# Performance work log

Measured on AMD Instinct MI355X. Metric: run time of the kernel, lower is better.

The kernel has to match this reference:

```python
import jax, jax.numpy as jnp
import numpy as np

EPS = 1e-08
SLOPE = 0.01  # LeakyReLU default negative_slope
B = 2097152
H = 32

def leaky_relu(x):
    return jnp.where(x >= 0, x, SLOPE * x)

def gram_schmidt(v, w):
    # v, w: [b,3]
    v_on = v / (jnp.linalg.norm(v, axis=-1, keepdims=True) + EPS)
    proj = jnp.sum(w * v_on, axis=-1, keepdims=True) * v_on
    w_orth = w - proj
    w_on = w_orth / (jnp.linalg.norm(w_orth, axis=-1, keepdims=True) + EPS)
    u_on = jnp.cross(v_on, w_on)
    R = jnp.stack((v_on, w_on, u_on), axis=-1)  # [b,3,3]
    v_local = jnp.einsum('bji,bj->bi', R, v)    # R^T @ v
    w_local = jnp.einsum('bji,bj->bi', R, w)
    return R, v_local, w_local

def setup_inputs() -> dict:
    key = jax.random.key(0)
    ks = jax.random.split(key, 12)
    std = 0.0001  # init_weights() normal std
    return {
        'v': jax.random.normal(ks[0], (B, 3), jnp.float32),
        'w': jax.random.normal(ks[1], (B, 3), jnp.float32),
        'W1': jax.random.normal(ks[2], (H, 3), jnp.float32) * std,
        'b1': jax.random.normal(ks[3], (H,), jnp.float32) * std,
        'W2': jax.random.normal(ks[4], (H, H), jnp.float32) * std,
        'b2': jax.random.normal(ks[5], (H,), jnp.float32) * std,
        'Wd1': jax.random.normal(ks[6], (H, H), jnp.float32) * std,
        'bd1': jax.random.normal(ks[7], (H,), jnp.float32) * std,
        'Wd2': jax.random.normal(ks[8], (3, H), jnp.float32) * std,
        'bd2': jax.random.normal(ks[9], (3,), jnp.float32) * std,
        'bias': jnp.array([[0.0, 0.0, -9.81]], jnp.float32),
    }

def reference(v, w, W1, b1, W2, b2, Wd1, bd1, Wd2, bd2, bias):
    shapes = v.shape
    b = shapes[0]
    v = v.reshape(b, 3)
    w = w.reshape(b, 3)
    R, v_local, w_local = gram_schmidt(v, w)
    feat = jnp.concatenate([v_local[..., :1], w_local[..., :2]], axis=-1)  # [b,3]
    h1 = leaky_relu(feat @ W1.T + b1)           # [b,H]
    h = leaky_relu(h1 @ W2.T + b2) * h1         # [b,H]
    y = leaky_relu(h @ Wd1.T + bd1) @ Wd2.T + bd2  # [b,3]
    y = jnp.einsum('bij,bj->bi', R, y) + bias
    return y.reshape(shapes)
```

## Files before the change

### kernel.cpp

```cpp
#include <hip/hip_runtime.h>
#include <math.h>

typedef __attribute__((ext_vector_type(8))) short short8;
typedef __attribute__((ext_vector_type(4))) float f32x4;
typedef __attribute__((ext_vector_type(4))) unsigned int u32x4;
typedef __attribute__((ext_vector_type(2))) unsigned long long u64x2;

static __device__ __forceinline__ unsigned int fbits(float f) {
    union { float f; unsigned int u; } v; v.f = f; return v.u;
}
static __device__ __forceinline__ float bitsf(unsigned int u) {
    union { float f; unsigned int u; } v; v.u = u; return v.f;
}
static __device__ __forceinline__ unsigned int pkbf(float lo, float hi) {
    return (fbits(hi) & 0xFFFF0000u) | (fbits(lo) >> 16);
}
static __device__ __forceinline__ float bflo(unsigned int u) { return bitsf(u << 16); }
static __device__ __forceinline__ float bfhi(unsigned int u) { return bitsf(u & 0xFFFF0000u); }
static __device__ __forceinline__ float leaky(float x) { return fmaxf(x, 0.01f * x); }


__global__ __launch_bounds__(256, 4) void aero_mfma(
    const float* __restrict__ vin, const float* __restrict__ win,
    const float* __restrict__ gW1, const float* __restrict__ gb1,
    const float* __restrict__ gW2, const float* __restrict__ gb2,
    const float* __restrict__ gWd1, const float* __restrict__ gbd1,
    const float* __restrict__ gWd2, const float* __restrict__ gbd2,
    const float* __restrict__ gbias,
    float* __restrict__ out, int nrows)
{
    __shared__ unsigned long long hbuf[256 * 9];
    __shared__ unsigned long long zbuf[256 * 9];
    unsigned int* const z32 = (unsigned int*)zbuf;

    const int tid = threadIdx.x;
    int row = blockIdx.x * 256 + tid;
    if (row >= nrows) row = nrows - 1;

    const int i15   = tid & 15;
    const int quad  = (tid >> 4) & 3;
    const int wbase = tid & 192;

    unsigned int bw2[2][4], bwd1[2][4];
    float b2v[2], bd1v[2];
    #pragma unroll
    for (int u = 0; u < 2; ++u) {
        const int n = u * 16 + i15;
        const float* p2 = gW2  + n * 32 + 4 * quad;
        const float* p3 = gWd1 + n * 32 + 4 * quad;
        #pragma unroll
        for (int j = 0; j < 4; ++j) {
            bw2[u][j]  = pkbf(p2[j], p2[j + 16]);
            bwd1[u][j] = pkbf(p3[j], p3[j + 16]);
        }
        b2v[u]  = gb2[n];
        bd1v[u] = gbd1[n];
    }

    const float v0 = vin[3 * row + 0], v1 = vin[3 * row + 1], v2 = vin[3 * row + 2];
    const float w0 = win[3 * row + 0], w1 = win[3 * row + 1], w2 = win[3 * row + 2];

    const float nv  = sqrtf(v0 * v0 + v1 * v1 + v2 * v2) + 1e-8f;
    const float rnv = 1.0f / nv;
    const float a0 = v0 * rnv, a1 = v1 * rnv, a2 = v2 * rnv;
    const float proj = w0 * a0 + w1 * a1 + w2 * a2;
    const float o0 = w0 - proj * a0, o1 = w1 - proj * a1, o2 = w2 - proj * a2;
    const float nw  = sqrtf(o0 * o0 + o1 * o1 + o2 * o2) + 1e-8f;
    const float rnw = 1.0f / nw;
    const float c0 = o0 * rnw, c1 = o1 * rnw, c2 = o2 * rnw;
    const float u0 = a1 * c2 - a2 * c1;
    const float u1 = a2 * c0 - a0 * c2;
    const float u2 = a0 * c1 - a1 * c0;

    const float f0 = v0 * a0 + v1 * a1 + v2 * a2;
    const float f1 = proj;
    const float f2 = w0 * c0 + w1 * c1 + w2 * c2;

    float h1[32];
    #pragma unroll
    for (int j = 0; j < 32; ++j) {
        float acc = gb1[j];
        acc = fmaf(gW1[3 * j + 0], f0, acc);
        acc = fmaf(gW1[3 * j + 1], f1, acc);
        acc = fmaf(gW1[3 * j + 2], f2, acc);
        h1[j] = leaky(acc);
    }

    {
        unsigned long long* dst = hbuf + tid * 9;
        #pragma unroll
        for (int c2 = 0; c2 < 8; ++c2) {
            const unsigned int lo = pkbf(h1[2 * c2],     h1[2 * c2 + 16]);
            const unsigned int hi = pkbf(h1[2 * c2 + 1], h1[2 * c2 + 17]);
            dst[c2] = (unsigned long long)lo | ((unsigned long long)hi << 32);
        }
    }

    __syncthreads();
    {
        const short8 bf0 = __builtin_bit_cast(short8, (u32x4){bw2[0][0], bw2[0][1], bw2[0][2], bw2[0][3]});
        const short8 bf1 = __builtin_bit_cast(short8, (u32x4){bw2[1][0], bw2[1][1], bw2[1][2], bw2[1][3]});
        #pragma unroll
        for (int t = 0; t < 4; ++t) {
            const int ra = wbase + 16 * t + i15;
            u64x2 av;
            av.x = hbuf[ra * 9 + 2 * quad];
            av.y = hbuf[ra * 9 + 2 * quad + 1];
            const short8 af = __builtin_bit_cast(short8, av);
            f32x4 acc0 = {b2v[0], b2v[0], b2v[0], b2v[0]};
            f32x4 acc1 = {b2v[1], b2v[1], b2v[1], b2v[1]};
            acc0 = __builtin_amdgcn_mfma_f32_16x16x32_bf16(af, bf0, acc0, 0, 0, 0);
            acc1 = __builtin_amdgcn_mfma_f32_16x16x32_bf16(af, bf1, acc1, 0, 0, 0);
            const int zr = wbase + 16 * t + 4 * quad;
            #pragma unroll
            for (int r = 0; r < 4; ++r)
                z32[(zr + r) * 18 + i15] = pkbf(acc0[r], acc1[r]);
        }
    }

    __syncthreads();
    {
        const unsigned long long* src = zbuf + tid * 9;
        unsigned long long* dst = hbuf + tid * 9;
        #pragma unroll
        for (int c2 = 0; c2 < 8; ++c2) {
            const unsigned long long zz = src[c2];
            const unsigned int ulo = (unsigned int)zz;
            const unsigned int uhi = (unsigned int)(zz >> 32);
            const float g0 = leaky(bflo(ulo)) * h1[2 * c2];
            const float g1 = leaky(bfhi(ulo)) * h1[2 * c2 + 16];
            const float g2 = leaky(bflo(uhi)) * h1[2 * c2 + 1];
            const float g3 = leaky(bfhi(uhi)) * h1[2 * c2 + 17];
            const unsigned int lo = pkbf(g0, g1);
            const unsigned int hi = pkbf(g2, g3);
            dst[c2] = (unsigned long long)lo | ((unsigned long long)hi << 32);
        }
    }

    __syncthreads();
    {
        const short8 bf0 = __builtin_bit_cast(short8, (u32x4){bwd1[0][0], bwd1[0][1], bwd1[0][2], bwd1[0][3]});
        const short8 bf1 = __builtin_bit_cast(short8, (u32x4){bwd1[1][0], bwd1[1][1], bwd1[1][2], bwd1[1][3]});
        #pragma unroll
        for (int t = 0; t < 4; ++t) {
            const int ra = wbase + 16 * t + i15;
            u64x2 av;
            av.x = hbuf[ra * 9 + 2 * quad];
            av.y = hbuf[ra * 9 + 2 * quad + 1];
            const short8 af = __builtin_bit_cast(short8, av);
            f32x4 acc0 = {bd1v[0], bd1v[0], bd1v[0], bd1v[0]};
            f32x4 acc1 = {bd1v[1], bd1v[1], bd1v[1], bd1v[1]};
            acc0 = __builtin_amdgcn_mfma_f32_16x16x32_bf16(af, bf0, acc0, 0, 0, 0);
            acc1 = __builtin_amdgcn_mfma_f32_16x16x32_bf16(af, bf1, acc1, 0, 0, 0);
            const int zr = wbase + 16 * t + 4 * quad;
            #pragma unroll
            for (int r = 0; r < 4; ++r)
                z32[(zr + r) * 18 + i15] = pkbf(acc0[r], acc1[r]);
        }
    }

    __syncthreads();
    {
        const unsigned long long* src = zbuf + tid * 9;
        float h3[32];
        #pragma unroll
        for (int c2 = 0; c2 < 8; ++c2) {
            const unsigned long long zz = src[c2];
            const unsigned int ulo = (unsigned int)zz;
            const unsigned int uhi = (unsigned int)(zz >> 32);
            h3[2 * c2]      = leaky(bflo(ulo));
            h3[2 * c2 + 16] = leaky(bfhi(ulo));
            h3[2 * c2 + 1]  = leaky(bflo(uhi));
            h3[2 * c2 + 17] = leaky(bfhi(uhi));
        }

        float y0 = gbd2[0], y1 = gbd2[1], y2 = gbd2[2];
        #pragma unroll
        for (int k = 0; k < 32; ++k) {
            y0 = fmaf(gWd2[0 * 32 + k], h3[k], y0);
            y1 = fmaf(gWd2[1 * 32 + k], h3[k], y1);
            y2 = fmaf(gWd2[2 * 32 + k], h3[k], y2);
        }

        out[3 * row + 0] = fmaf(a0, y0, fmaf(c0, y1, fmaf(u0, y2, gbias[0])));
        out[3 * row + 1] = fmaf(a1, y0, fmaf(c1, y1, fmaf(u1, y2, gbias[1])));
        out[3 * row + 2] = fmaf(a2, y0, fmaf(c2, y1, fmaf(u2, y2, gbias[2])));
    }
}

extern "C" void kernel_launch(void* const* d_in, const int* in_sizes, int n_in,
                              void* d_out, int out_size, void* d_ws, size_t ws_size,
                              hipStream_t stream) {
    const float* v    = (const float*)d_in[0];
    const float* w    = (const float*)d_in[1];
    const float* W1   = (const float*)d_in[2];
    const float* b1   = (const float*)d_in[3];
    const float* W2   = (const float*)d_in[4];
    const float* b2   = (const float*)d_in[5];
    const float* Wd1  = (const float*)d_in[6];
    const float* bd1  = (const float*)d_in[7];
    const float* Wd2  = (const float*)d_in[8];
    const float* bd2  = (const float*)d_in[9];
    const float* bias = (const float*)d_in[10];

    const int nrows = in_sizes[0] / 3;
    dim3 block(256);
    dim3 grid((nrows + 255) / 256);
    hipLaunchKernelGGL(aero_mfma, grid, block, 0, stream,
                       v, w, W1, b1, W2, b2, Wd1, bd1, Wd2, bd2, bias,
                       (float*)d_out, nrows);
}
```

Measured before the change: 141.7 us.

## Move all four MLP layers onto MFMA and fuse activations into epilogues

```diff
diff --git a/kernel.cpp b/kernel.cpp
--- a/kernel.cpp
+++ b/kernel.cpp
@@ -1,5 +1,4 @@
 #include <hip/hip_runtime.h>
-#include <math.h>
 
 typedef __attribute__((ext_vector_type(8))) short short8;
 typedef __attribute__((ext_vector_type(4))) float f32x4;
@@ -13,11 +12,15 @@
     union { float f; unsigned int u; } v; v.u = u; return v.f;
 }
 static __device__ __forceinline__ unsigned int pkbf(float lo, float hi) {
-    return (fbits(hi) & 0xFFFF0000u) | (fbits(lo) >> 16);
+    return __builtin_amdgcn_perm(fbits(hi), fbits(lo), 0x07060302u);
 }
 static __device__ __forceinline__ float bflo(unsigned int u) { return bitsf(u << 16); }
 static __device__ __forceinline__ float bfhi(unsigned int u) { return bitsf(u & 0xFFFF0000u); }
 static __device__ __forceinline__ float leaky(float x) { return fmaxf(x, 0.01f * x); }
+static __device__ __forceinline__ float rsqrt_nr(float x) {
+    const float r = __builtin_amdgcn_rsqf(x);
+    return r * (1.5f - (0.5f * x) * (r * r));
+}
 
 
 __global__ __launch_bounds__(256, 4) void aero_mfma(
@@ -31,7 +34,10 @@
 {
     __shared__ unsigned long long hbuf[256 * 9];
     __shared__ unsigned long long zbuf[256 * 9];
-    unsigned int* const z32 = (unsigned int*)zbuf;
+    __shared__ u32x4 fybuf[256];
+    unsigned int* const h32  = (unsigned int*)hbuf;
+    unsigned int* const z32  = (unsigned int*)zbuf;
+    unsigned int* const fy32 = (unsigned int*)fybuf;
 
     const int tid = threadIdx.x;
     int row = blockIdx.x * 256 + tid;
@@ -41,8 +47,8 @@
     const int quad  = (tid >> 4) & 3;
     const int wbase = tid & 192;
 
-    unsigned int bw2[2][4], bwd1[2][4];
-    float b2v[2], bd1v[2];
+    unsigned int bw1[2][4], bw2[2][4], bwd1[2][4], bwd2[4];
+    float b1v[2], b2v[2], bd1v[2];
     #pragma unroll
     for (int u = 0; u < 2; ++u) {
         const int n = u * 16 + i15;
@@ -50,56 +56,73 @@
         const float* p3 = gWd1 + n * 32 + 4 * quad;
         #pragma unroll
         for (int j = 0; j < 4; ++j) {
+            float l1 = 0.0f;
+            if (quad == 0 && j < 3) l1 = gW1[n * 3 + j];
+            bw1[u][j]  = fbits(l1) >> 16;
             bw2[u][j]  = pkbf(p2[j], p2[j + 16]);
             bwd1[u][j] = pkbf(p3[j], p3[j + 16]);
         }
+        b1v[u]  = gb1[n];
         b2v[u]  = gb2[n];
         bd1v[u] = gbd1[n];
     }
+    #pragma unroll
+    for (int j = 0; j < 4; ++j) {
+        float lo = 0.0f, hi = 0.0f;
+        if (i15 < 3) {
+            const float* p4 = gWd2 + i15 * 32 + 4 * quad;
+            lo = p4[j]; hi = p4[j + 16];
+        }
+        bwd2[j] = pkbf(lo, hi);
+    }
+    const float bd2v = (i15 < 3) ? gbd2[i15] : 0.0f;
 
     const float v0 = vin[3 * row + 0], v1 = vin[3 * row + 1], v2 = vin[3 * row + 2];
     const float w0 = win[3 * row + 0], w1 = win[3 * row + 1], w2 = win[3 * row + 2];
 
-    const float nv  = sqrtf(v0 * v0 + v1 * v1 + v2 * v2) + 1e-8f;
-    const float rnv = 1.0f / nv;
-    const float a0 = v0 * rnv, a1 = v1 * rnv, a2 = v2 * rnv;
-    const float proj = w0 * a0 + w1 * a1 + w2 * a2;
-    const float o0 = w0 - proj * a0, o1 = w1 - proj * a1, o2 = w2 - proj * a2;
-    const float nw  = sqrtf(o0 * o0 + o1 * o1 + o2 * o2) + 1e-8f;
-    const float rnw = 1.0f / nw;
-    const float c0 = o0 * rnw, c1 = o1 * rnw, c2 = o2 * rnw;
-    const float u0 = a1 * c2 - a2 * c1;
-    const float u1 = a2 * c0 - a0 * c2;
-    const float u2 = a0 * c1 - a1 * c0;
-
-    const float f0 = v0 * a0 + v1 * a1 + v2 * a2;
+    const float sv  = v0 * v0 + v1 * v1 + v2 * v2;
+    const float rnv = rsqrt_nr(sv);
+    const float vo0 = v0 * rnv, vo1 = v1 * rnv, vo2 = v2 * rnv;
+    const float proj = w0 * vo0 + w1 * vo1 + w2 * vo2;
+    const float o0 = w0 - proj * vo0, o1 = w1 - proj * vo1, o2 = w2 - proj * vo2;
+    const float sw  = o0 * o0 + o1 * o1 + o2 * o2;
+    const float rnw = rsqrt_nr(sw);
+    const float wo0 = o0 * rnw, wo1 = o1 * rnw, wo2 = o2 * rnw;
+    const float uo0 = vo1 * wo2 - vo2 * wo1;
+    const float uo1 = vo2 * wo0 - vo0 * wo2;
+    const float uo2 = vo0 * wo1 - vo1 * wo0;
+
+    const float f0 = sv * rnv;
     const float f1 = proj;
-    const float f2 = w0 * c0 + w1 * c1 + w2 * c2;
-
-    float h1[32];
-    #pragma unroll
-    for (int j = 0; j < 32; ++j) {
-        float acc = gb1[j];
-        acc = fmaf(gW1[3 * j + 0], f0, acc);
-        acc = fmaf(gW1[3 * j + 1], f1, acc);
-        acc = fmaf(gW1[3 * j + 2], f2, acc);
-        h1[j] = leaky(acc);
-    }
-
-    {
-        unsigned long long* dst = hbuf + tid * 9;
-        #pragma unroll
-        for (int c2 = 0; c2 < 8; ++c2) {
-            const unsigned int lo = pkbf(h1[2 * c2],     h1[2 * c2 + 16]);
-            const unsigned int hi = pkbf(h1[2 * c2 + 1], h1[2 * c2 + 17]);
-            dst[c2] = (unsigned long long)lo | ((unsigned long long)hi << 32);
-        }
-    }
-
-    __syncthreads();
+    const float f2 = sw * rnw;
+
+    fybuf[tid] = (u32x4){ fbits(f0) >> 16, fbits(f1) >> 16, fbits(f2) >> 16, 0u };
+    __syncthreads();
+
+    {
+        const short8 bf0 = __builtin_bit_cast(short8, (u32x4){bw1[0][0], bw1[0][1], bw1[0][2], bw1[0][3]});
+        const short8 bf1 = __builtin_bit_cast(short8, (u32x4){bw1[1][0], bw1[1][1], bw1[1][2], bw1[1][3]});
+        const f32x4 cb0 = {b1v[0], b1v[0], b1v[0], b1v[0]};
+        const f32x4 cb1 = {b1v[1], b1v[1], b1v[1], b1v[1]};
+        #pragma unroll
+        for (int t = 0; t < 4; ++t) {
+            const int ra = wbase + 16 * t + i15;
+            const short8 af = __builtin_bit_cast(short8, fybuf[ra]);
+            const f32x4 acc0 = __builtin_amdgcn_mfma_f32_16x16x32_bf16(af, bf0, cb0, 0, 0, 0);
+            const f32x4 acc1 = __builtin_amdgcn_mfma_f32_16x16x32_bf16(af, bf1, cb1, 0, 0, 0);
+            const int zr = wbase + 16 * t + 4 * quad;
+            #pragma unroll
+            for (int r = 0; r < 4; ++r)
+                h32[(zr + r) * 18 + i15] = pkbf(leaky(acc0[r]), leaky(acc1[r]));
+        }
+    }
+    __syncthreads();
+
     {
         const short8 bf0 = __builtin_bit_cast(short8, (u32x4){bw2[0][0], bw2[0][1], bw2[0][2], bw2[0][3]});
         const short8 bf1 = __builtin_bit_cast(short8, (u32x4){bw2[1][0], bw2[1][1], bw2[1][2], bw2[1][3]});
+        const f32x4 cb0 = {b2v[0], b2v[0], b2v[0], b2v[0]};
+        const f32x4 cb1 = {b2v[1], b2v[1], b2v[1], b2v[1]};
         #pragma unroll
         for (int t = 0; t < 4; ++t) {
             const int ra = wbase + 16 * t + i15;
@@ -107,40 +130,44 @@
             av.x = hbuf[ra * 9 + 2 * quad];
             av.y = hbuf[ra * 9 + 2 * quad + 1];
             const short8 af = __builtin_bit_cast(short8, av);
-            f32x4 acc0 = {b2v[0], b2v[0], b2v[0], b2v[0]};
-            f32x4 acc1 = {b2v[1], b2v[1], b2v[1], b2v[1]};
-            acc0 = __builtin_amdgcn_mfma_f32_16x16x32_bf16(af, bf0, acc0, 0, 0, 0);
-            acc1 = __builtin_amdgcn_mfma_f32_16x16x32_bf16(af, bf1, acc1, 0, 0, 0);
+            const f32x4 acc0 = __builtin_amdgcn_mfma_f32_16x16x32_bf16(af, bf0, cb0, 0, 0, 0);
+            const f32x4 acc1 = __builtin_amdgcn_mfma_f32_16x16x32_bf16(af, bf1, cb1, 0, 0, 0);
+            const int zr = wbase + 16 * t + 4 * quad;
+            #pragma unroll
+            for (int r = 0; r < 4; ++r) {
+                const unsigned int g = h32[(zr + r) * 18 + i15];
+                z32[(zr + r) * 18 + i15] =
+                    pkbf(leaky(acc0[r]) * bflo(g), leaky(acc1[r]) * bfhi(g));
+            }
+        }
+    }
+    __syncthreads();
+
+    {
+        const short8 bf0 = __builtin_bit_cast(short8, (u32x4){bwd1[0][0], bwd1[0][1], bwd1[0][2], bwd1[0][3]});
+        const short8 bf1 = __builtin_bit_cast(short8, (u32x4){bwd1[1][0], bwd1[1][1], bwd1[1][2], bwd1[1][3]});
+        const f32x4 cb0 = {bd1v[0], bd1v[0], bd1v[0], bd1v[0]};
+        const f32x4 cb1 = {bd1v[1], bd1v[1], bd1v[1], bd1v[1]};
+        #pragma unroll
+        for (int t = 0; t < 4; ++t) {
+            const int ra = wbase + 16 * t + i15;
+            u64x2 av;
+            av.x = zbuf[ra * 9 + 2 * quad];
+            av.y = zbuf[ra * 9 + 2 * quad + 1];
+            const short8 af = __builtin_bit_cast(short8, av);
+            const f32x4 acc0 = __builtin_amdgcn_mfma_f32_16x16x32_bf16(af, bf0, cb0, 0, 0, 0);
+            const f32x4 acc1 = __builtin_amdgcn_mfma_f32_16x16x32_bf16(af, bf1, cb1, 0, 0, 0);
             const int zr = wbase + 16 * t + 4 * quad;
             #pragma unroll
             for (int r = 0; r < 4; ++r)
-                z32[(zr + r) * 18 + i15] = pkbf(acc0[r], acc1[r]);
-        }
-    }
-
-    __syncthreads();
-    {
-        const unsigned long long* src = zbuf + tid * 9;
-        unsigned long long* dst = hbuf + tid * 9;
-        #pragma unroll
-        for (int c2 = 0; c2 < 8; ++c2) {
-            const unsigned long long zz = src[c2];
-            const unsigned int ulo = (unsigned int)zz;
-            const unsigned int uhi = (unsigned int)(zz >> 32);
-            const float g0 = leaky(bflo(ulo)) * h1[2 * c2];
-            const float g1 = leaky(bfhi(ulo)) * h1[2 * c2 + 16];
-            const float g2 = leaky(bflo(uhi)) * h1[2 * c2 + 1];
-            const float g3 = leaky(bfhi(uhi)) * h1[2 * c2 + 17];
-            const unsigned int lo = pkbf(g0, g1);
-            const unsigned int hi = pkbf(g2, g3);
-            dst[c2] = (unsigned long long)lo | ((unsigned long long)hi << 32);
-        }
-    }
-
-    __syncthreads();
-    {
-        const short8 bf0 = __builtin_bit_cast(short8, (u32x4){bwd1[0][0], bwd1[0][1], bwd1[0][2], bwd1[0][3]});
-        const short8 bf1 = __builtin_bit_cast(short8, (u32x4){bwd1[1][0], bwd1[1][1], bwd1[1][2], bwd1[1][3]});
+                h32[(zr + r) * 18 + i15] = pkbf(leaky(acc0[r]), leaky(acc1[r]));
+        }
+    }
+    __syncthreads();
+
+    {
+        const short8 bfE = __builtin_bit_cast(short8, (u32x4){bwd2[0], bwd2[1], bwd2[2], bwd2[3]});
+        const f32x4 cbE = {bd2v, bd2v, bd2v, bd2v};
         #pragma unroll
         for (int t = 0; t < 4; ++t) {
             const int ra = wbase + 16 * t + i15;
@@ -148,43 +175,23 @@
             av.x = hbuf[ra * 9 + 2 * quad];
             av.y = hbuf[ra * 9 + 2 * quad + 1];
             const short8 af = __builtin_bit_cast(short8, av);
-            f32x4 acc0 = {bd1v[0], bd1v[0], bd1v[0], bd1v[0]};
-            f32x4 acc1 = {bd1v[1], bd1v[1], bd1v[1], bd1v[1]};
-            acc0 = __builtin_amdgcn_mfma_f32_16x16x32_bf16(af, bf0, acc0, 0, 0, 0);
-            acc1 = __builtin_amdgcn_mfma_f32_16x16x32_bf16(af, bf1, acc1, 0, 0, 0);
-            const int zr = wbase + 16 * t + 4 * quad;
-            #pragma unroll
-            for (int r = 0; r < 4; ++r)
-                z32[(zr + r) * 18 + i15] = pkbf(acc0[r], acc1[r]);
-        }
-    }
-
-    __syncthreads();
-    {
-        const unsigned long long* src = zbuf + tid * 9;
-        float h3[32];
-        #pragma unroll
-        for (int c2 = 0; c2 < 8; ++c2) {
-            const unsigned long long zz = src[c2];
-            const unsigned int ulo = (unsigned int)zz;
-            const unsigned int uhi = (unsigned int)(zz >> 32);
-            h3[2 * c2]      = leaky(bflo(ulo));
-            h3[2 * c2 + 16] = leaky(bfhi(ulo));
-            h3[2 * c2 + 1]  = leaky(bflo(uhi));
-            h3[2 * c2 + 17] = leaky(bfhi(uhi));
-        }
-
-        float y0 = gbd2[0], y1 = gbd2[1], y2 = gbd2[2];
-        #pragma unroll
-        for (int k = 0; k < 32; ++k) {
-            y0 = fmaf(gWd2[0 * 32 + k], h3[k], y0);
-            y1 = fmaf(gWd2[1 * 32 + k], h3[k], y1);
-            y2 = fmaf(gWd2[2 * 32 + k], h3[k], y2);
-        }
-
-        out[3 * row + 0] = fmaf(a0, y0, fmaf(c0, y1, fmaf(u0, y2, gbias[0])));
-        out[3 * row + 1] = fmaf(a1, y0, fmaf(c1, y1, fmaf(u1, y2, gbias[1])));
-        out[3 * row + 2] = fmaf(a2, y0, fmaf(c2, y1, fmaf(u2, y2, gbias[2])));
+            const f32x4 accE = __builtin_amdgcn_mfma_f32_16x16x32_bf16(af, bfE, cbE, 0, 0, 0);
+            const int zr = wbase + 16 * t + 4 * quad;
+            if (i15 < 3) {
+                #pragma unroll
+                for (int r = 0; r < 4; ++r)
+                    fy32[(zr + r) * 4 + i15] = fbits(accE[r]);
+            }
+        }
+    }
+    __syncthreads();
+
+    {
+        const u32x4 yv = fybuf[tid];
+        const float y0 = bitsf(yv.x), y1 = bitsf(yv.y), y2 = bitsf(yv.z);
+        out[3 * row + 0] = fmaf(vo0, y0, fmaf(wo0, y1, fmaf(uo0, y2, gbias[0])));
+        out[3 * row + 1] = fmaf(vo1, y0, fmaf(wo1, y1, fmaf(uo1, y2, gbias[1])));
+        out[3 * row + 2] = fmaf(vo2, y0, fmaf(wo2, y1, fmaf(uo2, y2, gbias[2])));
     }
 }
 
```

Measured after the change: 197.9 us. +39.6%, slower.

## Fuse layer-2 activation into MFMA epilogue, use rsqrt and byte-perm packing

Applied to the files above, without the earlier changes.

```diff
diff --git a/kernel.cpp b/kernel.cpp
--- a/kernel.cpp
+++ b/kernel.cpp
@@ -1,5 +1,4 @@
 #include <hip/hip_runtime.h>
-#include <math.h>
 
 typedef __attribute__((ext_vector_type(8))) short short8;
 typedef __attribute__((ext_vector_type(4))) float f32x4;
@@ -13,11 +12,15 @@
     union { float f; unsigned int u; } v; v.u = u; return v.f;
 }
 static __device__ __forceinline__ unsigned int pkbf(float lo, float hi) {
-    return (fbits(hi) & 0xFFFF0000u) | (fbits(lo) >> 16);
+    return __builtin_amdgcn_perm(fbits(hi), fbits(lo), 0x07060302u);
 }
 static __device__ __forceinline__ float bflo(unsigned int u) { return bitsf(u << 16); }
 static __device__ __forceinline__ float bfhi(unsigned int u) { return bitsf(u & 0xFFFF0000u); }
 static __device__ __forceinline__ float leaky(float x) { return fmaxf(x, 0.01f * x); }
+static __device__ __forceinline__ float rsqrt_nr(float x) {
+    const float r = __builtin_amdgcn_rsqf(x);
+    return r * (1.5f - (0.5f * x) * (r * r));
+}
 
 
 __global__ __launch_bounds__(256, 4) void aero_mfma(
@@ -31,6 +34,7 @@
 {
     __shared__ unsigned long long hbuf[256 * 9];
     __shared__ unsigned long long zbuf[256 * 9];
+    unsigned int* const h32 = (unsigned int*)hbuf;
     unsigned int* const z32 = (unsigned int*)zbuf;
 
     const int tid = threadIdx.x;
@@ -60,21 +64,21 @@
     const float v0 = vin[3 * row + 0], v1 = vin[3 * row + 1], v2 = vin[3 * row + 2];
     const float w0 = win[3 * row + 0], w1 = win[3 * row + 1], w2 = win[3 * row + 2];
 
-    const float nv  = sqrtf(v0 * v0 + v1 * v1 + v2 * v2) + 1e-8f;
-    const float rnv = 1.0f / nv;
+    const float sv  = v0 * v0 + v1 * v1 + v2 * v2;
+    const float rnv = rsqrt_nr(sv);
     const float a0 = v0 * rnv, a1 = v1 * rnv, a2 = v2 * rnv;
     const float proj = w0 * a0 + w1 * a1 + w2 * a2;
     const float o0 = w0 - proj * a0, o1 = w1 - proj * a1, o2 = w2 - proj * a2;
-    const float nw  = sqrtf(o0 * o0 + o1 * o1 + o2 * o2) + 1e-8f;
-    const float rnw = 1.0f / nw;
+    const float sw  = o0 * o0 + o1 * o1 + o2 * o2;
+    const float rnw = rsqrt_nr(sw);
     const float c0 = o0 * rnw, c1 = o1 * rnw, c2 = o2 * rnw;
     const float u0 = a1 * c2 - a2 * c1;
     const float u1 = a2 * c0 - a0 * c2;
     const float u2 = a0 * c1 - a1 * c0;
 
-    const float f0 = v0 * a0 + v1 * a1 + v2 * a2;
+    const float f0 = sv * rnv;
     const float f1 = proj;
-    const float f2 = w0 * c0 + w1 * c1 + w2 * c2;
+    const float f2 = sw * rnw;
 
     float h1[32];
     #pragma unroll
@@ -100,6 +104,8 @@
     {
         const short8 bf0 = __builtin_bit_cast(short8, (u32x4){bw2[0][0], bw2[0][1], bw2[0][2], bw2[0][3]});
         const short8 bf1 = __builtin_bit_cast(short8, (u32x4){bw2[1][0], bw2[1][1], bw2[1][2], bw2[1][3]});
+        const f32x4 cb0 = {b2v[0], b2v[0], b2v[0], b2v[0]};
+        const f32x4 cb1 = {b2v[1], b2v[1], b2v[1], b2v[1]};
         #pragma unroll
         for (int t = 0; t < 4; ++t) {
             const int ra = wbase + 16 * t + i15;
@@ -107,61 +113,43 @@
             av.x = hbuf[ra * 9 + 2 * quad];
             av.y = hbuf[ra * 9 + 2 * quad + 1];
             const short8 af = __builtin_bit_cast(short8, av);
-            f32x4 acc0 = {b2v[0], b2v[0], b2v[0], b2v[0]};
-            f32x4 acc1 = {b2v[1], b2v[1], b2v[1], b2v[1]};
-            acc0 = __builtin_amdgcn_mfma_f32_16x16x32_bf16(af, bf0, acc0, 0, 0, 0);
-            acc1 = __builtin_amdgcn_mfma_f32_16x16x32_bf16(af, bf1, acc1, 0, 0, 0);
+            const f32x4 acc0 = __builtin_amdgcn_mfma_f32_16x16x32_bf16(af, bf0, cb0, 0, 0, 0);
+            const f32x4 acc1 = __builtin_amdgcn_mfma_f32_16x16x32_bf16(af, bf1, cb1, 0, 0, 0);
+            const int zr = wbase + 16 * t + 4 * quad;
+            #pragma unroll
+            for (int r = 0; r < 4; ++r) {
+                const unsigned int g = h32[(zr + r) * 18 + i15];
+                z32[(zr + r) * 18 + i15] =
+                    pkbf(leaky(acc0[r]) * bflo(g), leaky(acc1[r]) * bfhi(g));
+            }
+        }
+    }
+
+    __syncthreads();
+    {
+        const short8 bf0 = __builtin_bit_cast(short8, (u32x4){bwd1[0][0], bwd1[0][1], bwd1[0][2], bwd1[0][3]});
+        const short8 bf1 = __builtin_bit_cast(short8, (u32x4){bwd1[1][0], bwd1[1][1], bwd1[1][2], bwd1[1][3]});
+        const f32x4 cb0 = {bd1v[0], bd1v[0], bd1v[0], bd1v[0]};
+        const f32x4 cb1 = {bd1v[1], bd1v[1], bd1v[1], bd1v[1]};
+        #pragma unroll
+        for (int t = 0; t < 4; ++t) {
+            const int ra = wbase + 16 * t + i15;
+            u64x2 av;
+            av.x = zbuf[ra * 9 + 2 * quad];
+            av.y = zbuf[ra * 9 + 2 * quad + 1];
+            const short8 af = __builtin_bit_cast(short8, av);
+            const f32x4 acc0 = __builtin_amdgcn_mfma_f32_16x16x32_bf16(af, bf0, cb0, 0, 0, 0);
+            const f32x4 acc1 = __builtin_amdgcn_mfma_f32_16x16x32_bf16(af, bf1, cb1, 0, 0, 0);
             const int zr = wbase + 16 * t + 4 * quad;
             #pragma unroll
             for (int r = 0; r < 4; ++r)
-                z32[(zr + r) * 18 + i15] = pkbf(acc0[r], acc1[r]);
+                h32[(zr + r) * 18 + i15] = pkbf(acc0[r], acc1[r]);
         }
     }
 
     __syncthreads();
     {
-        const unsigned long long* src = zbuf + tid * 9;
-        unsigned long long* dst = hbuf + tid * 9;
-        #pragma unroll
-        for (int c2 = 0; c2 < 8; ++c2) {
-            const unsigned long long zz = src[c2];
-            const unsigned int ulo = (unsigned int)zz;
-            const unsigned int uhi = (unsigned int)(zz >> 32);
-            const float g0 = leaky(bflo(ulo)) * h1[2 * c2];
-            const float g1 = leaky(bfhi(ulo)) * h1[2 * c2 + 16];
-            const float g2 = leaky(bflo(uhi)) * h1[2 * c2 + 1];
-            const float g3 = leaky(bfhi(uhi)) * h1[2 * c2 + 17];
-            const unsigned int lo = pkbf(g0, g1);
-            const unsigned int hi = pkbf(g2, g3);
-            dst[c2] = (unsigned long long)lo | ((unsigned long long)hi << 32);
-        }
-    }
-
-    __syncthreads();
-    {
-        const short8 bf0 = __builtin_bit_cast(short8, (u32x4){bwd1[0][0], bwd1[0][1], bwd1[0][2], bwd1[0][3]});
-        const short8 bf1 = __builtin_bit_cast(short8, (u32x4){bwd1[1][0], bwd1[1][1], bwd1[1][2], bwd1[1][3]});
-        #pragma unroll
-        for (int t = 0; t < 4; ++t) {
-            const int ra = wbase + 16 * t + i15;
-            u64x2 av;
-            av.x = hbuf[ra * 9 + 2 * quad];
-            av.y = hbuf[ra * 9 + 2 * quad + 1];
-            const short8 af = __builtin_bit_cast(short8, av);
-            f32x4 acc0 = {bd1v[0], bd1v[0], bd1v[0], bd1v[0]};
-            f32x4 acc1 = {bd1v[1], bd1v[1], bd1v[1], bd1v[1]};
-            acc0 = __builtin_amdgcn_mfma_f32_16x16x32_bf16(af, bf0, acc0, 0, 0, 0);
-            acc1 = __builtin_amdgcn_mfma_f32_16x16x32_bf16(af, bf1, acc1, 0, 0, 0);
-            const int zr = wbase + 16 * t + 4 * quad;
-            #pragma unroll
-            for (int r = 0; r < 4; ++r)
-                z32[(zr + r) * 18 + i15] = pkbf(acc0[r], acc1[r]);
-        }
-    }
-
-    __syncthreads();
-    {
-        const unsigned long long* src = zbuf + tid * 9;
+        const unsigned long long* src = hbuf + tid * 9;
         float h3[32];
         #pragma unroll
         for (int c2 = 0; c2 < 8; ++c2) {
```

Result: no change. 140.6 us (-0.8%).
